# Performance work log

Hardware: AMD Instinct MI355X
Metric: run time of the kernel (lower is better)

The kernel has to match this reference:

```python
import jax, jax.numpy as jnp
import numpy as np

N = 100000   # nodes
E = 400000   # edges
G = 1024     # graphs in batch
IN = 4; H = 128; HD = 4; DH = H // HD; L = 3; ED = 4; FF = 2 * H; JK = H * L
SCALE = 1.0 / np.sqrt(DH).astype(np.float32)


def _ln(x, g, b):
    m = x.mean(-1, keepdims=True)
    v = x.var(-1, keepdims=True)
    return (x - m) / jnp.sqrt(v + 1e-5) * g + b


def setup_inputs() -> dict:
    key = jax.random.key(0)
    ks = jax.random.split(key, 24)
    rn = lambda k, s, sc=0.05: jax.random.normal(k, s, jnp.float32) * sc
    return {
        "x": rn(ks[0], (N, IN), 1.0),
        "edge_index": jax.random.randint(ks[1], (2, E), 0, N),
        "edge_attr": rn(ks[2], (E, ED), 1.0),
        "batch": jnp.sort(jax.random.randint(ks[3], (N,), 0, G)),
        "u": rn(ks[4], (G, 1), 1.0),
        "Win": rn(ks[5], (IN, H)), "b_in": jnp.zeros(H),
        "Wq": rn(ks[6], (L, H, H)), "bq": jnp.zeros((L, H)),
        "Wk": rn(ks[7], (L, H, H)), "bk": jnp.zeros((L, H)),
        "Wv": rn(ks[8], (L, H, H)), "bv": jnp.zeros((L, H)),
        "We": rn(ks[9], (L, ED, H)),
        "Wskip": rn(ks[10], (L, H, H)), "bskip": jnp.zeros((L, H)),
        "ln1_g": jnp.ones((L, H)), "ln1_b": jnp.zeros((L, H)),
        "Wf1": rn(ks[11], (L, H, FF)), "bf1": jnp.zeros((L, FF)),
        "Wf2": rn(ks[12], (L, FF, H)), "bf2": jnp.zeros((L, H)),
        "ln2_g": jnp.ones((L, H)), "ln2_b": jnp.zeros((L, H)),
        "Wg1": rn(ks[13], (JK, H)), "bg1": jnp.zeros(H),
        "Wg2": rn(ks[14], (H, 1)), "bg2": jnp.zeros(1),
        "Wh1": rn(ks[15], (JK + 1, H)), "bh1": jnp.zeros(H),
        "Wh2": rn(ks[16], (H, 3)), "bh2": jnp.zeros(3),
    }


def reference(x, edge_index, edge_attr, batch, u,
              Win, b_in, Wq, bq, Wk, bk, Wv, bv, We, Wskip, bskip,
              ln1_g, ln1_b, Wf1, bf1, Wf2, bf2, ln2_g, ln2_b,
              Wg1, bg1, Wg2, bg2, Wh1, bh1, Wh2, bh2):
    src, dst = edge_index[0], edge_index[1]
    h = x @ Win + b_in                                   # [N,H]
    xs = []
    for l in range(L):
        q = (h @ Wq[l] + bq[l]).reshape(N, HD, DH)
        k_n = h @ Wk[l] + bk[l]
        v_n = h @ Wv[l] + bv[l]
        e = edge_attr @ We[l]                            # [E,H] edge bias
        ke = (k_n[src] + e).reshape(E, HD, DH)
        ve = (v_n[src] + e).reshape(E, HD, DH)
        logits = (q[dst] * ke).sum(-1) * SCALE           # [E,HD]
        m = jax.ops.segment_max(logits, dst, N)
        p = jnp.exp(logits - m[dst])
        s = jax.ops.segment_sum(p, dst, N)
        alpha = p / (s[dst] + 1e-16)                     # segment softmax per dst node
        agg = jax.ops.segment_sum(alpha[:, :, None] * ve, dst, N).reshape(N, H)
        attn = agg + h @ Wskip[l] + bskip[l]             # root weight (skip lin)
        h = _ln(h + attn, ln1_g[l], ln1_b[l])
        ff = jax.nn.relu(h @ Wf1[l] + bf1[l]) @ Wf2[l] + bf2[l]
        h = _ln(h + ff, ln2_g[l], ln2_b[l])
        xs.append(h)
    xc = jnp.concatenate(xs, -1)                         # JumpingKnowledge 'cat' [N,JK]
    gate = (jax.nn.relu(xc @ Wg1 + bg1) @ Wg2 + bg2)[:, 0]  # [N]
    gm = jax.ops.segment_max(gate, batch, G)
    gp = jnp.exp(gate - gm[batch])
    gs = jax.ops.segment_sum(gp, batch, G)
    w = gp / (gs[batch] + 1e-16)                         # per-graph softmax
    pooled = jax.ops.segment_sum(w[:, None] * xc, batch, G)  # [G,JK]
    out = jnp.concatenate([pooled, u], 1)                # [G,JK+1]
    return jax.nn.relu(out @ Wh1 + bh1) @ Wh2 + bh2      # [G,3]
```

## Files before the change

### kernel.cpp

```cpp
#include <hip/hip_runtime.h>
#include <math.h>

#define H 128
#define LAYERS 3
#define FFDIM 256
#define JK 384
#define ATT_SCALE 0.17677669529663687f

typedef unsigned short u16;
typedef __attribute__((ext_vector_type(4))) float f32x4;
typedef __attribute__((ext_vector_type(8))) short short8;
typedef __attribute__((ext_vector_type(8))) unsigned short ushort8v;

static inline int cdiv(int a, int b) { return (a + b - 1) / b; }

static __device__ __forceinline__ float bf2f(u16 u) {
    union { unsigned int i; float f; } v; v.i = ((unsigned int)u) << 16; return v.f;
}
static __device__ __forceinline__ u16 f2bf(float f) {
    union { float f; unsigned int i; } v; v.f = f;
    unsigned int r = v.i + 0x7FFFu + ((v.i >> 16) & 1u);
    return (u16)(r >> 16);
}

__global__ void hist_kernel(const int* __restrict__ ei, int* __restrict__ counts, int E) {
    int e = blockIdx.x * blockDim.x + threadIdx.x;
    if (e >= E) return;
    atomicAdd(&counts[ei[E + e]], 1);
}

__global__ __launch_bounds__(256) void scan1_kernel(const int* __restrict__ counts,
                                                    int* __restrict__ offsets,
                                                    int* __restrict__ bsum, int N) {
    __shared__ int sh[256];
    int t = threadIdx.x;
    int base = blockIdx.x * 1024 + t * 4;
    int v0 = 0, v1 = 0, v2 = 0, v3 = 0;
    if (base + 3 < N) {
        int4 q = *(const int4*)&counts[base];
        v0 = q.x; v1 = q.y; v2 = q.z; v3 = q.w;
    } else {
        if (base < N) v0 = counts[base];
        if (base + 1 < N) v1 = counts[base + 1];
        if (base + 2 < N) v2 = counts[base + 2];
        if (base + 3 < N) v3 = counts[base + 3];
    }
    int ts = v0 + v1 + v2 + v3;
    sh[t] = ts; __syncthreads();
    for (int off = 1; off < 256; off <<= 1) {
        int x = (t >= off) ? sh[t - off] : 0;
        __syncthreads(); sh[t] += x; __syncthreads();
    }
    int excl = sh[t] - ts;
    if (base < N)     offsets[base]     = excl;
    if (base + 1 < N) offsets[base + 1] = excl + v0;
    if (base + 2 < N) offsets[base + 2] = excl + v0 + v1;
    if (base + 3 < N) offsets[base + 3] = excl + v0 + v1 + v2;
    if (t == 255) bsum[blockIdx.x] = sh[255];
}

__global__ __launch_bounds__(128) void scan2_kernel(const int* __restrict__ bsum,
                                                    int* __restrict__ boffs,
                                                    int* __restrict__ offsets, int nb, int N) {
    __shared__ int sh[128];
    int t = threadIdx.x;
    int s = (t < nb) ? bsum[t] : 0;
    sh[t] = s; __syncthreads();
    for (int off = 1; off < 128; off <<= 1) {
        int x = (t >= off) ? sh[t - off] : 0;
        __syncthreads(); sh[t] += x; __syncthreads();
    }
    if (t < nb) boffs[t] = sh[t] - s;
    if (t == 0) offsets[N] = sh[nb - 1];
}

__global__ __launch_bounds__(256) void scan3_kernel(int* __restrict__ offsets,
                                                    const int* __restrict__ boffs, int N) {
    int add = boffs[blockIdx.x];
    int base = blockIdx.x * 1024 + threadIdx.x * 4;
#pragma unroll
    for (int i = 0; i < 4; ++i)
        if (base + i < N) offsets[base + i] += add;
}

__global__ void scatter_kernel(const int* __restrict__ ei, const float* __restrict__ eattr,
                               const int* __restrict__ offsets,
                               int* __restrict__ cursor, int* __restrict__ psrc,
                               float4* __restrict__ pe, int E) {
    int e = blockIdx.x * blockDim.x + threadIdx.x;
    if (e >= E) return;
    int d = ei[E + e];
    int pos = atomicAdd(&cursor[d], 1);
    int o = offsets[d] + pos;
    psrc[o] = ei[e];
    pe[o] = *(const float4*)&eattr[(size_t)e * 4];
}

__global__ __launch_bounds__(256) void dhist_kernel(const int* __restrict__ counts,
                                                    int* __restrict__ dhist, int N) {
    __shared__ int lh[64];
    int t = threadIdx.x;
    if (t < 64) lh[t] = 0;
    __syncthreads();
    int n = blockIdx.x * 256 + t;
    if (n < N) atomicAdd(&lh[min(counts[n], 63)], 1);
    __syncthreads();
    if (t < 64 && lh[t]) atomicAdd(&dhist[t], lh[t]);
}

__global__ __launch_bounds__(64) void dscan_kernel(const int* __restrict__ dhist,
                                                   int* __restrict__ dcur) {
    __shared__ int sh[64];
    int t = threadIdx.x;
    int s = dhist[t];
    sh[t] = s; __syncthreads();
    for (int off = 1; off < 64; off <<= 1) {
        int x = (t >= off) ? sh[t - off] : 0;
        __syncthreads(); sh[t] += x; __syncthreads();
    }
    dcur[t] = sh[t] - s;
}

__global__ __launch_bounds__(256) void dscatter_kernel(const int* __restrict__ counts,
                                                       int* __restrict__ dcur,
                                                       int* __restrict__ nperm, int N) {
    __shared__ int lh[64], lbase[64];
    int t = threadIdx.x;
    if (t < 64) lh[t] = 0;
    __syncthreads();
    int n = blockIdx.x * 256 + t;
    int b = 0, rank = 0;
    if (n < N) {
        b = min(counts[n], 63);
        rank = atomicAdd(&lh[b], 1);
    }
    __syncthreads();
    if (t < 64 && lh[t]) lbase[t] = atomicAdd(&dcur[t], lh[t]);
    __syncthreads();
    if (n < N) nperm[lbase[b] + rank] = n;
}

__global__ void graph_bounds_kernel(const int* __restrict__ batch, int* __restrict__ gstart,
                                    int N, int G) {
    int g = blockIdx.x * blockDim.x + threadIdx.x;
    if (g > G) return;
    int lo = 0, hi = N;
    while (lo < hi) { int mid = (lo + hi) >> 1; if (batch[mid] < g) lo = mid + 1; else hi = mid; }
    gstart[g] = lo;
}

struct TD { const float* src; int dstoff, K, N; };
struct TA { TD d[19]; };

__global__ __launch_bounds__(256) void wconv_kernel(TA a, u16* __restrict__ WT) {
    TD d = a.d[blockIdx.y];
    int i = blockIdx.x * 256 + threadIdx.x;
    int tot = d.K * d.N;
    if (i >= tot) return;
    int c = i / d.K, k = i - c * d.K;
    WT[d.dstoff + i] = f2bf(d.src[(size_t)k * d.N + c]);
}

__global__ __launch_bounds__(256) void input_proj_kernel(const float* __restrict__ x,
                                                         const float* __restrict__ Win,
                                                         const float* __restrict__ b_in,
                                                         u16* __restrict__ h, int ldh, int N) {
    int idx = blockIdx.x * 256 + threadIdx.x;
    int n = idx >> 6, c = (idx & 63) * 2;
    if (n >= N) return;
    float4 xv = *(const float4*)&x[(size_t)n * 4];
    float o0 = b_in[c]     + xv.x * Win[c]     + xv.y * Win[H + c]     + xv.z * Win[2 * H + c]     + xv.w * Win[3 * H + c];
    float o1 = b_in[c + 1] + xv.x * Win[c + 1] + xv.y * Win[H + c + 1] + xv.z * Win[2 * H + c + 1] + xv.w * Win[3 * H + c + 1];
    ushort2 s; s.x = f2bf(o0); s.y = f2bf(o1);
    *(ushort2*)&h[(size_t)n * ldh + c] = s;
}

__device__ __forceinline__ void stage_tile(const u16* __restrict__ g, int ld, int row0,
                                           int nrows, int kt, u16* __restrict__ sm, int t) {
#pragma unroll
    for (int i = 0; i < 4; ++i) {
        int f = i * 256 + t;
        int row = f >> 3, ck = f & 7;
        int n = row0 + row; if (n >= nrows) n = nrows - 1;
        uint4 v = *(const uint4*)(g + (size_t)n * ld + kt + ck * 8);
        int sw = ck ^ (row & 7);
        *(uint4*)(sm + row * 64 + sw * 8) = v;
    }
}

template <int MODE, int NBY>
__global__ __launch_bounds__(256) void gemm_mfma(
    const u16* __restrict__ A, int lda,
    const u16* __restrict__ WT, int K,
    const float* __restrict__ b0, const float* __restrict__ b1,
    const float* __restrict__ b2, const float* __restrict__ b3,
    u16* __restrict__ obf, u16* __restrict__ obf2, float* __restrict__ of32,
    int nrows)
{
    alignas(16) __shared__ char smemraw[33792];
    u16* Asm = (u16*)smemraw;
    u16* Bsm = (u16*)(smemraw + 16384);
    float* stage = (float*)smemraw;
    int t = threadIdx.x;
    int lane = t & 63, wid = t >> 6;
    int wr = wid >> 1, wc = wid & 1;

    int T = gridDim.x, id = blockIdx.x;
    int qd = T >> 3, rr = T & 7;
    int xcd = id & 7, pos = id >> 3;
    int swz = (xcd < rr ? xcd * (qd + 1) : rr * (qd + 1) + (xcd - rr) * qd) + pos;
    int by = swz & (NBY - 1);
    int row0 = (swz / NBY) * 128;

    const u16* WTb = WT + (size_t)by * 128 * K;

    f32x4 acc[4][4] = {};

    for (int kt = 0; kt < K; kt += 64) {
        stage_tile(A, lda, row0, nrows, kt, Asm, t);
        stage_tile(WTb, K, 0, 128, kt, Bsm, t);
        __syncthreads();
        int g = lane >> 4;
        int l15 = lane & 15;
#pragma unroll
        for (int kk = 0; kk < 2; ++kk) {
            int cb = kk * 4 + g;
            short8 af[4], bf[4];
#pragma unroll
            for (int mi = 0; mi < 4; ++mi) {
                int r = wr * 64 + mi * 16 + l15;
                af[mi] = *(const short8*)(Asm + r * 64 + ((cb ^ (r & 7)) * 8));
            }
#pragma unroll
            for (int nj = 0; nj < 4; ++nj) {
                int c = wc * 64 + nj * 16 + l15;
                bf[nj] = *(const short8*)(Bsm + c * 64 + ((cb ^ (c & 7)) * 8));
            }
#pragma unroll
            for (int mi = 0; mi < 4; ++mi)
#pragma unroll
                for (int nj = 0; nj < 4; ++nj)
                    acc[mi][nj] = __builtin_amdgcn_mfma_f32_16x16x32_bf16(af[mi], bf[nj], acc[mi][nj], 0, 0, 0);
        }
        __syncthreads();
    }

    int g = lane >> 4, l15 = lane & 15;

    if (MODE == 3) {
        float* gsum = (float*)Asm;
        float part[4][4];
#pragma unroll
        for (int mi = 0; mi < 4; ++mi)
#pragma unroll
            for (int r = 0; r < 4; ++r) part[mi][r] = 0.f;
#pragma unroll
        for (int nj = 0; nj < 4; ++nj) {
            int col = wc * 64 + nj * 16 + l15;
            float bb = b0[col];
            float w2 = b1[col];
#pragma unroll
            for (int mi = 0; mi < 4; ++mi)
#pragma unroll
                for (int r = 0; r < 4; ++r) {
                    float v = fmaxf(acc[mi][nj][r] + bb, 0.f);
                    part[mi][r] = fmaf(v, w2, part[mi][r]);
                }
        }
#pragma unroll
        for (int off = 1; off <= 8; off <<= 1)
#pragma unroll
            for (int mi = 0; mi < 4; ++mi)
#pragma unroll
                for (int r = 0; r < 4; ++r) part[mi][r] += __shfl_xor(part[mi][r], off);
        if (wc == 0 && l15 == 0) {
#pragma unroll
            for (int mi = 0; mi < 4; ++mi)
#pragma unroll
                for (int r = 0; r < 4; ++r)
                    gsum[wr * 64 + mi * 16 + g * 4 + r] = part[mi][r];
        }
        __syncthreads();
        if (wc == 1 && l15 == 0) {
            float bg2v = b2[0];
#pragma unroll
            for (int mi = 0; mi < 4; ++mi)
#pragma unroll
                for (int r = 0; r < 4; ++r) {
                    int lr = wr * 64 + mi * 16 + g * 4 + r;
                    int n = row0 + lr;
                    if (n < nrows) of32[n] = part[mi][r] + gsum[lr] + bg2v;
                }
        }
        return;
    }

    const float* bias = (by == 0) ? b0 : (by == 1) ? b1 : (by == 2) ? b2 : b3;
    u16* ob; int ldob;
    if (by < 3) { ob = obf + by * 128; ldob = 384; }
    else { ob = obf2; ldob = 128; }

#pragma unroll
    for (int p = 0; p < 2; ++p) {
        if (wr == p) {
#pragma unroll
            for (int nj = 0; nj < 4; ++nj) {
                int col = wc * 64 + nj * 16 + l15;
                float bb = bias[col];
#pragma unroll
                for (int mi = 0; mi < 4; ++mi)
#pragma unroll
                    for (int r = 0; r < 4; ++r)
                        stage[(mi * 16 + g * 4 + r) * 132 + col] = acc[mi][nj][r] + bb;
            }
        }
        __syncthreads();
#pragma unroll
        for (int it = 0; it < 4; ++it) {
            int lr = it * 16 + (t >> 4);
            int gr = row0 + p * 64 + lr;
            if (gr < nrows) {
                int c8 = (t & 15) * 8;
                ushort8v o;
                if (by == 3) {
                    ushort8v hv = *(const ushort8v*)&A[(size_t)gr * lda + c8];
#pragma unroll
                    for (int i = 0; i < 8; ++i) o[i] = f2bf(stage[lr * 132 + c8 + i] + bf2f(hv[i]));
                } else {
#pragma unroll
                    for (int i = 0; i < 8; ++i) o[i] = f2bf(stage[lr * 132 + c8 + i]);
                }
                *(ushort8v*)&ob[(size_t)gr * ldob + c8] = o;
            }
        }
        __syncthreads();
    }
}

__global__ __launch_bounds__(256) void ff_fused(
    const u16* __restrict__ qkv,
    const u16* __restrict__ W1T,
    const u16* __restrict__ W2T,
    const float* __restrict__ bias1,
    const float* __restrict__ bias2,
    const float* __restrict__ g2, const float* __restrict__ b2v,
    u16* __restrict__ xcout,
    int nrows)
{
    alignas(16) __shared__ char smem[57344];
    u16* ff1s = (u16*)smem;
    u16* ast  = (u16*)(smem + 32768);
    u16* bst  = (u16*)(smem + 40960);
    float* stage = (float*)smem;

    int t = threadIdx.x;
    int lane = t & 63, wid = t >> 6;
    int wr = wid >> 1, wc = wid & 1;
    int g = lane >> 4, l15 = lane & 15;

    int T = gridDim.x, id = blockIdx.x;
    int qd = T >> 3, rr = T & 7;
    int xcd = id & 7, pos = id >> 3;
    int swz = (xcd < rr ? xcd * (qd + 1) : rr * (qd + 1) + (xcd - rr) * qd) + pos;
    int row0 = swz * 64;

    for (int ch = 0; ch < 2; ++ch) {
        f32x4 acc[2][4] = {};
        for (int kt = 0; kt < 128; kt += 64) {
#pragma unroll
            for (int i = 0; i < 2; ++i) {
                int f = i * 256 + t;
                int row = f >> 3, ck = f & 7;
                int n = row0 + row; if (n >= nrows) n = nrows - 1;
                uint4 v = *(const uint4*)(qkv + (size_t)n * 384 + kt + ck * 8);
                *(uint4*)(ast + row * 64 + ((ck ^ (row & 7)) * 8)) = v;
            }
#pragma unroll
            for (int i = 0; i < 4; ++i) {
                int f = i * 256 + t;
                int row = f >> 3, ck = f & 7;
                uint4 v = *(const uint4*)(W1T + (size_t)(ch * 128 + row) * 128 + kt + ck * 8);
                *(uint4*)(bst + row * 64 + ((ck ^ (row & 7)) * 8)) = v;
            }
            __syncthreads();
#pragma unroll
            for (int kk = 0; kk < 2; ++kk) {
                int cb = kk * 4 + g;
                short8 af[2], bf[4];
#pragma unroll
                for (int mi = 0; mi < 2; ++mi) {
                    int r = wr * 32 + mi * 16 + l15;
                    af[mi] = *(const short8*)(ast + r * 64 + ((cb ^ (r & 7)) * 8));
                }
#pragma unroll
                for (int nj = 0; nj < 4; ++nj) {
                    int c = wc * 64 + nj * 16 + l15;
                    bf[nj] = *(const short8*)(bst + c * 64 + ((cb ^ (c & 7)) * 8));
                }
#pragma unroll
                for (int mi = 0; mi < 2; ++mi)
#pragma unroll
                    for (int nj = 0; nj < 4; ++nj)
                        acc[mi][nj] = __builtin_amdgcn_mfma_f32_16x16x32_bf16(af[mi], bf[nj], acc[mi][nj], 0, 0, 0);
            }
            __syncthreads();
        }
#pragma unroll
        for (int nj = 0; nj < 4; ++nj) {
            int col = ch * 128 + wc * 64 + nj * 16 + l15;
            float bb = bias1[col];
            int cb2 = col >> 3, j = col & 7;
#pragma unroll
            for (int mi = 0; mi < 2; ++mi)
#pragma unroll
                for (int r = 0; r < 4; ++r) {
                    int row = wr * 32 + mi * 16 + g * 4 + r;
                    float v = fmaxf(acc[mi][nj][r] + bb, 0.f);
                    int sc = (cb2 & 24) | ((cb2 & 7) ^ (row & 7));
                    ff1s[row * 256 + sc * 8 + j] = f2bf(v);
                }
        }
    }

    f32x4 acc2[2][4] = {};
    for (int kt2 = 0; kt2 < 256; kt2 += 64) {
#pragma unroll
        for (int i = 0; i < 4; ++i) {
            int f = i * 256 + t;
            int row = f >> 3, ck = f & 7;
            uint4 v = *(const uint4*)(W2T + (size_t)row * 256 + kt2 + ck * 8);
            *(uint4*)(bst + row * 64 + ((ck ^ (row & 7)) * 8)) = v;
        }
        __syncthreads();
#pragma unroll
        for (int kk = 0; kk < 2; ++kk) {
            int cb = kk * 4 + g;
            short8 af[2], bf[4];
#pragma unroll
            for (int mi = 0; mi < 2; ++mi) {
                int r = wr * 32 + mi * 16 + l15;
                int sc = (kt2 >> 3) | (cb ^ (r & 7));
                af[mi] = *(const short8*)(ff1s + r * 256 + sc * 8);
            }
#pragma unroll
            for (int nj = 0; nj < 4; ++nj) {
                int c = wc * 64 + nj * 16 + l15;
                bf[nj] = *(const short8*)(bst + c * 64 + ((cb ^ (c & 7)) * 8));
            }
#pragma unroll
            for (int mi = 0; mi < 2; ++mi)
#pragma unroll
                for (int nj = 0; nj < 4; ++nj)
                    acc2[mi][nj] = __builtin_amdgcn_mfma_f32_16x16x32_bf16(af[mi], bf[nj], acc2[mi][nj], 0, 0, 0);
        }
        __syncthreads();
    }

#pragma unroll
    for (int nj = 0; nj < 4; ++nj) {
        int col = wc * 64 + nj * 16 + l15;
        float bb = bias2[col];
#pragma unroll
        for (int mi = 0; mi < 2; ++mi)
#pragma unroll
            for (int r = 0; r < 4; ++r) {
                int row = wr * 32 + mi * 16 + g * 4 + r;
                stage[row * 132 + col] = acc2[mi][nj][r] + bb;
            }
    }
    __syncthreads();
    int sub2 = t & 15, rowg = t >> 4;
#pragma unroll
    for (int it = 0; it < 4; ++it) {
        int lr = it * 16 + rowg;
        int gr = row0 + lr;
        bool ok = gr < nrows;
        int c8 = sub2 * 8;
        float tv[8]; float sum = 0.f, sq = 0.f;
        if (ok) {
            ushort8v rv = *(const ushort8v*)&qkv[(size_t)gr * 384 + c8];
#pragma unroll
            for (int i = 0; i < 8; ++i) {
                tv[i] = stage[lr * 132 + c8 + i] + bf2f(rv[i]);
                sum += tv[i]; sq += tv[i] * tv[i];
            }
        }
#pragma unroll
        for (int off = 1; off <= 8; off <<= 1) { sum += __shfl_xor(sum, off); sq += __shfl_xor(sq, off); }
        if (ok) {
            float mean = sum * (1.f / 128.f);
            float var = sq * (1.f / 128.f) - mean * mean;
            float rstd = rsqrtf(var + 1e-5f);
            ushort8v o;
#pragma unroll
            for (int i = 0; i < 8; ++i)
                o[i] = f2bf((tv[i] - mean) * rstd * g2[c8 + i] + b2v[c8 + i]);
            *(ushort8v*)&xcout[(size_t)gr * 384 + c8] = o;
        }
    }
}

__global__ __launch_bounds__(256) void attn_kernel(
    u16* __restrict__ qkv,
    const u16* __restrict__ skipb,
    const int* __restrict__ offsets,
    const int* __restrict__ nperm,
    const int* __restrict__ psrc, const float4* __restrict__ pe,
    const float* __restrict__ We_l,
    const float* __restrict__ g1, const float* __restrict__ b1,
    int N)
{
    int tid = threadIdx.x;
    int grp = tid >> 4;
    int sub = tid & 15;
    int idx = blockIdx.x * 16 + grp;
    if (idx >= N) return;
    int n = nperm[idx];
    int d0 = sub * 8;

    float we[4][8];
#pragma unroll
    for (int aa = 0; aa < 4; ++aa) {
        float4 w0 = *(const float4*)&We_l[aa * H + d0];
        float4 w1 = *(const float4*)&We_l[aa * H + d0 + 4];
        we[aa][0] = w0.x; we[aa][1] = w0.y; we[aa][2] = w0.z; we[aa][3] = w0.w;
        we[aa][4] = w1.x; we[aa][5] = w1.y; we[aa][6] = w1.z; we[aa][7] = w1.w;
    }

    ushort8v qraw = *(const ushort8v*)&qkv[(size_t)n * JK + d0];
    float qf[8];
#pragma unroll
    for (int i = 0; i < 8; ++i) qf[i] = bf2f(qraw[i]);

    float qe[4];
#pragma unroll
    for (int aa = 0; aa < 4; ++aa) {
        float s = 0.f;
#pragma unroll
        for (int i = 0; i < 8; ++i) s = fmaf(qf[i], we[aa][i], s);
        s += __shfl_xor(s, 1);
        s += __shfl_xor(s, 2);
        qe[aa] = s;
    }

    float m0 = -INFINITY, ss0 = 0.f, m1 = -INFINITY, ss1 = 0.f;
    float a0[8] = {}, a1[8] = {};
    float w0a = 0.f, w0b = 0.f, w0c = 0.f, w0d = 0.f;
    float w1a = 0.f, w1b = 0.f, w1c = 0.f, w1d = 0.f;
    int e0v = offsets[n], e1v = offsets[n + 1];
    int deg = e1v - e0v;
    int npairs = deg >> 1;

    if (npairs > 0) {
        int j0 = e0v;
        int sA = psrc[j0], sB = psrc[j0 + 1];
        float4 eaA = pe[j0], eaB = pe[j0 + 1];
        const u16* srA = qkv + (size_t)sA * JK;
        const u16* srB = qkv + (size_t)sB * JK;
        ushort8v krA = *(const ushort8v*)&srA[H + d0];
        ushort8v vrA = *(const ushort8v*)&srA[2 * H + d0];
        ushort8v krB = *(const ushort8v*)&srB[H + d0];
        ushort8v vrB = *(const ushort8v*)&srB[2 * H + d0];
        for (int it = 0; it < npairs; ++it) {
            float4 eaA2, eaB2; ushort8v krA2, vrA2, krB2, vrB2;
            if (it + 1 < npairs) {
                int jn = e0v + (it + 1) * 2;
                int sA2 = psrc[jn], sB2 = psrc[jn + 1];
                eaA2 = pe[jn]; eaB2 = pe[jn + 1];
                const u16* srA2 = qkv + (size_t)sA2 * JK;
                const u16* srB2 = qkv + (size_t)sB2 * JK;
                krA2 = *(const ushort8v*)&srA2[H + d0];
                vrA2 = *(const ushort8v*)&srA2[2 * H + d0];
                krB2 = *(const ushort8v*)&srB2[H + d0];
                vrB2 = *(const ushort8v*)&srB2[2 * H + d0];
            }
            float pA = 0.f, pB = 0.f;
#pragma unroll
            for (int i = 0; i < 8; ++i) {
                pA = fmaf(qf[i], bf2f(krA[i]), pA);
                pB = fmaf(qf[i], bf2f(krB[i]), pB);
            }
            pA += __shfl_xor(pA, 1); pB += __shfl_xor(pB, 1);
            pA += __shfl_xor(pA, 2); pB += __shfl_xor(pB, 2);
            float lgA = (pA + eaA.x * qe[0] + eaA.y * qe[1] + eaA.z * qe[2] + eaA.w * qe[3]) * ATT_SCALE;
            float lgB = (pB + eaB.x * qe[0] + eaB.y * qe[1] + eaB.z * qe[2] + eaB.w * qe[3]) * ATT_SCALE;
            float mnA = fmaxf(m0, lgA);
            float mnB = fmaxf(m1, lgB);
            float cA = __expf(m0 - mnA), cB = __expf(m1 - mnB);
            float pvA = __expf(lgA - mnA), pvB = __expf(lgB - mnB);
            ss0 = ss0 * cA + pvA;
            ss1 = ss1 * cB + pvB;
#pragma unroll
            for (int i = 0; i < 8; ++i) {
                a0[i] = a0[i] * cA + pvA * bf2f(vrA[i]);
                a1[i] = a1[i] * cB + pvB * bf2f(vrB[i]);
            }
            w0a = w0a * cA + pvA * eaA.x; w0b = w0b * cA + pvA * eaA.y;
            w0c = w0c * cA + pvA * eaA.z; w0d = w0d * cA + pvA * eaA.w;
            w1a = w1a * cB + pvB * eaB.x; w1b = w1b * cB + pvB * eaB.y;
            w1c = w1c * cB + pvB * eaB.z; w1d = w1d * cB + pvB * eaB.w;
            m0 = mnA; m1 = mnB;
            krA = krA2; vrA = vrA2; eaA = eaA2;
            krB = krB2; vrB = vrB2; eaB = eaB2;
        }
    }
    if (deg & 1) {
        int j = e1v - 1;
        int s = psrc[j];
        float4 ea = pe[j];
        const u16* sr = qkv + (size_t)s * JK;
        ushort8v kr = *(const ushort8v*)&sr[H + d0];
        ushort8v vr = *(const ushort8v*)&sr[2 * H + d0];
        float part = 0.f;
#pragma unroll
        for (int i = 0; i < 8; ++i) part = fmaf(qf[i], bf2f(kr[i]), part);
        part += __shfl_xor(part, 1);
        part += __shfl_xor(part, 2);
        float lg = (part + ea.x * qe[0] + ea.y * qe[1] + ea.z * qe[2] + ea.w * qe[3]) * ATT_SCALE;
        float mn = fmaxf(m0, lg);
        float c = __expf(m0 - mn);
        float pv = __expf(lg - mn);
        ss0 = ss0 * c + pv;
#pragma unroll
        for (int i = 0; i < 8; ++i) a0[i] = a0[i] * c + pv * bf2f(vr[i]);
        w0a = w0a * c + pv * ea.x; w0b = w0b * c + pv * ea.y;
        w0c = w0c * c + pv * ea.z; w0d = w0d * c + pv * ea.w;
        m0 = mn;
    }
    float mm = fmaxf(m0, m1);
    if (mm > -INFINITY) {
        float c0 = (m0 > -INFINITY) ? __expf(m0 - mm) : 0.f;
        float c1 = (m1 > -INFINITY) ? __expf(m1 - mm) : 0.f;
        ss0 = ss0 * c0 + ss1 * c1;
#pragma unroll
        for (int i = 0; i < 8; ++i) a0[i] = a0[i] * c0 + a1[i] * c1;
        w0a = w0a * c0 + w1a * c1; w0b = w0b * c0 + w1b * c1;
        w0c = w0c * c0 + w1c * c1; w0d = w0d * c0 + w1d * c1;
    }
    float inv = 1.f / (ss0 + 1e-16f);
#pragma unroll
    for (int i = 0; i < 8; ++i)
        a0[i] += w0a * we[0][i] + w0b * we[1][i] + w0c * we[2][i] + w0d * we[3][i];

    ushort8v skraw = *(const ushort8v*)&skipb[(size_t)n * H + d0];
    float tv[8], sum = 0.f, sq = 0.f;
#pragma unroll
    for (int i = 0; i < 8; ++i) {
        tv[i] = a0[i] * inv + bf2f(skraw[i]);
        sum += tv[i]; sq += tv[i] * tv[i];
    }
#pragma unroll
    for (int off = 1; off <= 8; off <<= 1) { sum += __shfl_xor(sum, off); sq += __shfl_xor(sq, off); }
    float mean = sum * (1.f / 128.f);
    float var = sq * (1.f / 128.f) - mean * mean;
    float rstd = rsqrtf(var + 1e-5f);
    float4 ga = *(const float4*)&g1[d0];
    float4 gb = *(const float4*)&g1[d0 + 4];
    float4 ba = *(const float4*)&b1[d0];
    float4 bb = *(const float4*)&b1[d0 + 4];
    float gg[8] = {ga.x, ga.y, ga.z, ga.w, gb.x, gb.y, gb.z, gb.w};
    float bbv[8] = {ba.x, ba.y, ba.z, ba.w, bb.x, bb.y, bb.z, bb.w};
    ushort8v obv;
#pragma unroll
    for (int i = 0; i < 8; ++i)
        obv[i] = f2bf((tv[i] - mean) * rstd * gg[i] + bbv[i]);
    *(ushort8v*)&qkv[(size_t)n * JK + d0] = obv;
}

#define PCH 512
__global__ __launch_bounds__(256) void pool_kernel(const float* __restrict__ gate,
                                                   const u16* __restrict__ xc,
                                                   const int* __restrict__ gstart,
                                                   const float* __restrict__ u,
                                                   float* __restrict__ pooled, int G) {
    int g = blockIdx.x;
    int t = threadIdx.x;
    int s0 = gstart[g], s1 = gstart[g + 1];
    __shared__ float red[256];
    __shared__ float w[PCH];
    float mx = -INFINITY;
    for (int i = s0 + t; i < s1; i += 256) mx = fmaxf(mx, gate[i]);
    red[t] = mx; __syncthreads();
    for (int off = 128; off; off >>= 1) { if (t < off) red[t] = fmaxf(red[t], red[t + off]); __syncthreads(); }
    float gm = red[0]; __syncthreads();
    float sm = 0.f;
    for (int i = s0 + t; i < s1; i += 256) sm += __expf(gate[i] - gm);
    red[t] = sm; __syncthreads();
    for (int off = 128; off; off >>= 1) { if (t < off) red[t] += red[t + off]; __syncthreads(); }
    float inv = 1.f / (red[0] + 1e-16f);
    float acc0 = 0.f, acc1 = 0.f;
    for (int base = s0; base < s1; base += PCH) {
        int cnt = min(PCH, s1 - base);
        __syncthreads();
        for (int i = t; i < cnt; i += 256) w[i] = __expf(gate[base + i] - gm) * inv;
        __syncthreads();
        for (int c = 0; c < cnt; ++c) {
            const u16* row = xc + (size_t)(base + c) * JK;
            float wc = w[c];
            acc0 = fmaf(wc, bf2f(row[t]), acc0);
            if (t < 128) acc1 = fmaf(wc, bf2f(row[t + 256]), acc1);
        }
    }
    pooled[(size_t)g * (JK + 1) + t] = acc0;
    if (t < 128) pooled[(size_t)g * (JK + 1) + t + 256] = acc1;
    if (t == 0) pooled[(size_t)g * (JK + 1) + JK] = u[g];
}

__global__ __launch_bounds__(128) void head_kernel(const float* __restrict__ pooled,
                                                   const float* __restrict__ Wh1,
                                                   const float* __restrict__ bh1,
                                                   const float* __restrict__ Wh2,
                                                   const float* __restrict__ bh2,
                                                   float* __restrict__ out, int G) {
    int g = blockIdx.x;
    int j = threadIdx.x;
    __shared__ float hid[128];
    float acc = bh1[j];
    const float* pr = pooled + (size_t)g * (JK + 1);
    for (int k = 0; k < JK + 1; ++k) acc = fmaf(pr[k], Wh1[(size_t)k * H + j], acc);
    hid[j] = fmaxf(acc, 0.f);
    __syncthreads();
    if (j < 3) {
        float o = bh2[j];
        for (int k = 0; k < H; ++k) o += hid[k] * Wh2[k * 3 + j];
        out[(size_t)g * 3 + j] = o;
    }
}

extern "C" void kernel_launch(void* const* d_in, const int* in_sizes, int n_in,
                              void* d_out, int out_size, void* d_ws, size_t ws_size,
                              hipStream_t stream) {
    const float* x     = (const float*)d_in[0];
    const int*   ei    = (const int*)d_in[1];
    const float* eattr = (const float*)d_in[2];
    const int*   batch = (const int*)d_in[3];
    const float* u     = (const float*)d_in[4];
    const float* Win   = (const float*)d_in[5];
    const float* b_in  = (const float*)d_in[6];
    const float* Wq    = (const float*)d_in[7];
    const float* bq    = (const float*)d_in[8];
    const float* Wk    = (const float*)d_in[9];
    const float* bk    = (const float*)d_in[10];
    const float* Wv    = (const float*)d_in[11];
    const float* bv    = (const float*)d_in[12];
    const float* We    = (const float*)d_in[13];
    const float* Wskip = (const float*)d_in[14];
    const float* bskip = (const float*)d_in[15];
    const float* ln1_g = (const float*)d_in[16];
    const float* ln1_b = (const float*)d_in[17];
    const float* Wf1   = (const float*)d_in[18];
    const float* bf1   = (const float*)d_in[19];
    const float* Wf2   = (const float*)d_in[20];
    const float* bf2   = (const float*)d_in[21];
    const float* ln2_g = (const float*)d_in[22];
    const float* ln2_b = (const float*)d_in[23];
    const float* Wg1   = (const float*)d_in[24];
    const float* bg1   = (const float*)d_in[25];
    const float* Wg2   = (const float*)d_in[26];
    const float* bg2   = (const float*)d_in[27];
    const float* Wh1   = (const float*)d_in[28];
    const float* bh1   = (const float*)d_in[29];
    const float* Wh2   = (const float*)d_in[30];
    const float* bh2   = (const float*)d_in[31];

    const int N = in_sizes[3];
    const int E = in_sizes[1] / 2;
    const int G = in_sizes[4];

    char* p = (char*)d_ws;
    auto alloc = [&](size_t bytes) { char* r = p; p += (bytes + 255) & ~(size_t)255; return r; };
    int*    counts  = (int*)alloc((size_t)N * 4);
    int*    cursor  = (int*)alloc((size_t)N * 4);
    int*    offsets = (int*)alloc((size_t)(N + 1) * 4);
    int*    psrc    = (int*)alloc((size_t)E * 4);
    float4* pe      = (float4*)alloc((size_t)E * 16);
    int*    nperm   = (int*)alloc((size_t)N * 4);
    int*    gstart  = (int*)alloc((size_t)(G + 1) * 4);
    int*    bsum    = (int*)alloc(128 * 4);
    int*    boffs   = (int*)alloc(128 * 4);
    int*    dhist   = (int*)alloc(64 * 4);
    int*    dcur    = (int*)alloc(64 * 4);
    float*  gate    = (float*)alloc((size_t)N * 4);
    float*  pooled  = (float*)alloc((size_t)G * (JK + 1) * 4);
    u16*    WT      = (u16*)alloc((size_t)442368 * 2);
    u16*    skipb   = (u16*)alloc((size_t)N * H * 2);
    u16*    xc      = (u16*)alloc((size_t)N * JK * 2);
    u16*    qkv     = (u16*)alloc((size_t)N * JK * 2);

    const int QKVS_OFF = 0;
    const int F1_OFF   = 3 * 65536;
    const int F2_OFF   = F1_OFF + 3 * 32768;
    const int G1_OFF   = F2_OFF + 3 * 32768;

    hipMemsetAsync(counts, 0, (size_t)N * 4, stream);
    hipMemsetAsync(cursor, 0, (size_t)N * 4, stream);
    hipMemsetAsync(dhist, 0, 64 * 4, stream);

    int eb = cdiv(E, 256);
    int nb = cdiv(N, 1024);
    int nthb = cdiv(N, 256);
    hist_kernel<<<eb, 256, 0, stream>>>(ei, counts, E);
    scan1_kernel<<<nb, 256, 0, stream>>>(counts, offsets, bsum, N);
    scan2_kernel<<<1, 128, 0, stream>>>(bsum, boffs, offsets, nb, N);
    scan3_kernel<<<nb, 256, 0, stream>>>(offsets, boffs, N);
    scatter_kernel<<<eb, 256, 0, stream>>>(ei, eattr, offsets, cursor, psrc, pe, E);
    dhist_kernel<<<nthb, 256, 0, stream>>>(counts, dhist, N);
    dscan_kernel<<<1, 64, 0, stream>>>(dhist, dcur);
    dscatter_kernel<<<nthb, 256, 0, stream>>>(counts, dcur, nperm, N);
    graph_bounds_kernel<<<cdiv(G + 1, 256), 256, 0, stream>>>(batch, gstart, N, G);

    TA ta;
    for (int l = 0; l < 3; ++l) {
        ta.d[l * 4 + 0] = { Wq    + (size_t)l * 16384, QKVS_OFF + l * 65536 + 0,     128, 128 };
        ta.d[l * 4 + 1] = { Wk    + (size_t)l * 16384, QKVS_OFF + l * 65536 + 16384, 128, 128 };
        ta.d[l * 4 + 2] = { Wv    + (size_t)l * 16384, QKVS_OFF + l * 65536 + 32768, 128, 128 };
        ta.d[l * 4 + 3] = { Wskip + (size_t)l * 16384, QKVS_OFF + l * 65536 + 49152, 128, 128 };
        ta.d[12 + l]    = { Wf1   + (size_t)l * 32768, F1_OFF   + l * 32768,         128, 256 };
        ta.d[15 + l]    = { Wf2   + (size_t)l * 32768, F2_OFF   + l * 32768,         256, 128 };
    }
    ta.d[18] = { Wg1, G1_OFF, 384, 128 };
    dim3 wg(cdiv(49152, 256), 19);
    wconv_kernel<<<wg, 256, 0, stream>>>(ta, WT);

    input_proj_kernel<<<cdiv(N * 64, 256), 256, 0, stream>>>(x, Win, b_in, xc, JK, N);

    int gb = cdiv(N, 128);
    int gb64 = cdiv(N, 64);
    int nb16 = cdiv(N, 16);
    for (int l = 0; l < LAYERS; ++l) {
        const u16* hin = xc + (size_t)((l == 0) ? 0 : (l - 1) * H);
        gemm_mfma<0, 4><<<gb * 4, 256, 0, stream>>>(
            hin, JK, WT + QKVS_OFF + (size_t)l * 65536, 128,
            bq + l * H, bk + l * H, bv + l * H, bskip + l * H,
            qkv, skipb, nullptr, N);
        attn_kernel<<<nb16, 256, 0, stream>>>(qkv, skipb, offsets, nperm, psrc, pe,
                                              We + (size_t)l * 4 * H, ln1_g + l * H, ln1_b + l * H,
                                              N);
        ff_fused<<<gb64, 256, 0, stream>>>(
            qkv, WT + F1_OFF + (size_t)l * 32768, WT + F2_OFF + (size_t)l * 32768,
            bf1 + (size_t)l * FFDIM, bf2 + (size_t)l * H,
            ln2_g + (size_t)l * H, ln2_b + (size_t)l * H,
            xc + (size_t)l * H, N);
    }

    gemm_mfma<3, 1><<<gb, 256, 0, stream>>>(
        xc, JK, WT + G1_OFF, JK,
        bg1, Wg2, bg2, nullptr,
        nullptr, nullptr, gate, N);
    pool_kernel<<<G, 256, 0, stream>>>(gate, xc, gstart, u, pooled, G);
    head_kernel<<<G, 128, 0, stream>>>(pooled, Wh1, bh1, Wh2, bh2, (float*)d_out, G);
}
```

Baseline: 609.9 us.

## Fuse Q/K/V/skip projections into one block per row tile reusing A

The QKV+skip GEMM now launches one block per 128-row tile that loads the full A tile (K=128) into shared memory once and loops over the four weight column blocks, instead of launching four blocks that each reload A. The skip residual is read from the staged shared A tile rather than global memory, and the epilogue staging buffer uses an XOR swizzle with vectorized float4 reads instead of padded scalar reads. The gate GEMM is split out into its own kernel. This cuts redundant A loads and the grid is four times smaller, which may reduce parallelism and latency hiding.

```diff
diff --git a/kernel.cpp b/kernel.cpp
--- a/kernel.cpp
+++ b/kernel.cpp
@@ -188,40 +188,139 @@
     }
 }
 
-template <int MODE, int NBY>
-__global__ __launch_bounds__(256) void gemm_mfma(
+__global__ __launch_bounds__(256) void qkvs_kernel(
     const u16* __restrict__ A, int lda,
-    const u16* __restrict__ WT, int K,
-    const float* __restrict__ b0, const float* __restrict__ b1,
-    const float* __restrict__ b2, const float* __restrict__ b3,
-    u16* __restrict__ obf, u16* __restrict__ obf2, float* __restrict__ of32,
-    int nrows)
+    const u16* __restrict__ WT,
+    const float* __restrict__ bq, const float* __restrict__ bk,
+    const float* __restrict__ bv, const float* __restrict__ bs,
+    u16* __restrict__ qkv, u16* __restrict__ skipb, int nrows)
 {
-    alignas(16) __shared__ char smemraw[33792];
-    u16* Asm = (u16*)smemraw;
-    u16* Bsm = (u16*)(smemraw + 16384);
-    float* stage = (float*)smemraw;
+    alignas(16) __shared__ u16 Asm[2][128 * 64];
+    alignas(16) __shared__ u16 Bsm[2][128 * 64];
+    float* stage = (float*)Bsm;
     int t = threadIdx.x;
     int lane = t & 63, wid = t >> 6;
     int wr = wid >> 1, wc = wid & 1;
+    int g = lane >> 4, l15 = lane & 15;
 
     int T = gridDim.x, id = blockIdx.x;
     int qd = T >> 3, rr = T & 7;
     int xcd = id & 7, pos = id >> 3;
     int swz = (xcd < rr ? xcd * (qd + 1) : rr * (qd + 1) + (xcd - rr) * qd) + pos;
-    int by = swz & (NBY - 1);
-    int row0 = (swz / NBY) * 128;
-
-    const u16* WTb = WT + (size_t)by * 128 * K;
+    int row0 = swz * 128;
+
+    stage_tile(A, lda, row0, nrows, 0,  Asm[0], t);
+    stage_tile(A, lda, row0, nrows, 64, Asm[1], t);
+
+    for (int by = 0; by < 4; ++by) {
+        const u16* WTb = WT + (size_t)by * 128 * 128;
+        stage_tile(WTb, 128, 0, 128, 0,  Bsm[0], t);
+        stage_tile(WTb, 128, 0, 128, 64, Bsm[1], t);
+        __syncthreads();
+
+        f32x4 acc[4][4] = {};
+#pragma unroll
+        for (int h = 0; h < 2; ++h) {
+#pragma unroll
+            for (int kk = 0; kk < 2; ++kk) {
+                int cb = kk * 4 + g;
+                short8 af[4], bf[4];
+#pragma unroll
+                for (int mi = 0; mi < 4; ++mi) {
+                    int r = wr * 64 + mi * 16 + l15;
+                    af[mi] = *(const short8*)(Asm[h] + r * 64 + ((cb ^ (r & 7)) * 8));
+                }
+#pragma unroll
+                for (int nj = 0; nj < 4; ++nj) {
+                    int c = wc * 64 + nj * 16 + l15;
+                    bf[nj] = *(const short8*)(Bsm[h] + c * 64 + ((cb ^ (c & 7)) * 8));
+                }
+#pragma unroll
+                for (int mi = 0; mi < 4; ++mi)
+#pragma unroll
+                    for (int nj = 0; nj < 4; ++nj)
+                        acc[mi][nj] = __builtin_amdgcn_mfma_f32_16x16x32_bf16(af[mi], bf[nj], acc[mi][nj], 0, 0, 0);
+            }
+        }
+        __syncthreads();
+
+        const float* bias = (by == 0) ? bq : (by == 1) ? bk : (by == 2) ? bv : bs;
+        u16* ob; int ldob;
+        if (by < 3) { ob = qkv + by * 128; ldob = 384; }
+        else { ob = skipb; ldob = 128; }
+
+#pragma unroll
+        for (int p = 0; p < 2; ++p) {
+            if (wr == p) {
+#pragma unroll
+                for (int nj = 0; nj < 4; ++nj) {
+                    int col = wc * 64 + nj * 16 + l15;
+                    float bb = bias[col];
+#pragma unroll
+                    for (int mi = 0; mi < 4; ++mi)
+#pragma unroll
+                        for (int r = 0; r < 4; ++r) {
+                            int lr = mi * 16 + g * 4 + r;
+                            stage[lr * 128 + (col ^ ((lr & 7) << 3))] = acc[mi][nj][r] + bb;
+                        }
+                }
+            }
+            __syncthreads();
+#pragma unroll
+            for (int it = 0; it < 4; ++it) {
+                int lr = it * 16 + (t >> 4);
+                int gr = row0 + p * 64 + lr;
+                if (gr < nrows) {
+                    int c8 = (t & 15) * 8;
+                    int sc = c8 ^ ((lr & 7) << 3);
+                    float4 va = *(float4*)&stage[lr * 128 + sc];
+                    float4 vb = *(float4*)&stage[lr * 128 + sc + 4];
+                    float vv[8] = {va.x, va.y, va.z, va.w, vb.x, vb.y, vb.z, vb.w};
+                    ushort8v o;
+                    if (by == 3) {
+                        int arow = p * 64 + lr;
+                        int cc = t & 15;
+                        int h2 = cc >> 3, ck = cc & 7;
+                        ushort8v hv = *(const ushort8v*)(Asm[h2] + arow * 64 + ((ck ^ (arow & 7)) * 8));
+#pragma unroll
+                        for (int i = 0; i < 8; ++i) o[i] = f2bf(vv[i] + bf2f(hv[i]));
+                    } else {
+#pragma unroll
+                        for (int i = 0; i < 8; ++i) o[i] = f2bf(vv[i]);
+                    }
+                    *(ushort8v*)&ob[(size_t)gr * ldob + c8] = o;
+                }
+            }
+            __syncthreads();
+        }
+    }
+}
+
+__global__ __launch_bounds__(256) void gate_kernel(
+    const u16* __restrict__ A, int lda,
+    const u16* __restrict__ WT, int K,
+    const float* __restrict__ bg1, const float* __restrict__ Wg2,
+    const float* __restrict__ bg2,
+    float* __restrict__ gate, int nrows)
+{
+    alignas(16) __shared__ u16 Asm[128 * 64];
+    alignas(16) __shared__ u16 Bsm[128 * 64];
+    int t = threadIdx.x;
+    int lane = t & 63, wid = t >> 6;
+    int wr = wid >> 1, wc = wid & 1;
+    int g = lane >> 4, l15 = lane & 15;
+
+    int T = gridDim.x, id = blockIdx.x;
+    int qd = T >> 3, rr = T & 7;
+    int xcd = id & 7, pos = id >> 3;
+    int swz = (xcd < rr ? xcd * (qd + 1) : rr * (qd + 1) + (xcd - rr) * qd) + pos;
+    int row0 = swz * 128;
 
     f32x4 acc[4][4] = {};
-
     for (int kt = 0; kt < K; kt += 64) {
         stage_tile(A, lda, row0, nrows, kt, Asm, t);
-        stage_tile(WTb, K, 0, 128, kt, Bsm, t);
+        stage_tile(WT, K, 0, 128, kt, Bsm, t);
         __syncthreads();
-        int g = lane >> 4;
-        int l15 = lane & 15;
 #pragma unroll
         for (int kk = 0; kk < 2; ++kk) {
             int cb = kk * 4 + g;
@@ -245,95 +344,49 @@
         __syncthreads();
     }
 
-    int g = lane >> 4, l15 = lane & 15;
-
-    if (MODE == 3) {
-        float* gsum = (float*)Asm;
-        float part[4][4];
+    float* gsum = (float*)Asm;
+    float part[4][4];
+#pragma unroll
+    for (int mi = 0; mi < 4; ++mi)
+#pragma unroll
+        for (int r = 0; r < 4; ++r) part[mi][r] = 0.f;
+#pragma unroll
+    for (int nj = 0; nj < 4; ++nj) {
+        int col = wc * 64 + nj * 16 + l15;
+        float bb = bg1[col];
+        float w2 = Wg2[col];
 #pragma unroll
         for (int mi = 0; mi < 4; ++mi)
 #pragma unroll
-            for (int r = 0; r < 4; ++r) part[mi][r] = 0.f;
-#pragma unroll
-        for (int nj = 0; nj < 4; ++nj) {
-            int col = wc * 64 + nj * 16 + l15;
-            float bb = b0[col];
-            float w2 = b1[col];
-#pragma unroll
-            for (int mi = 0; mi < 4; ++mi)
-#pragma unroll
-                for (int r = 0; r < 4; ++r) {
-                    float v = fmaxf(acc[mi][nj][r] + bb, 0.f);
-                    part[mi][r] = fmaf(v, w2, part[mi][r]);
-                }
-        }
-#pragma unroll
-        for (int off = 1; off <= 8; off <<= 1)
-#pragma unroll
-            for (int mi = 0; mi < 4; ++mi)
-#pragma unroll
-                for (int r = 0; r < 4; ++r) part[mi][r] += __shfl_xor(part[mi][r], off);
-        if (wc == 0 && l15 == 0) {
-#pragma unroll
-            for (int mi = 0; mi < 4; ++mi)
-#pragma unroll
-                for (int r = 0; r < 4; ++r)
-                    gsum[wr * 64 + mi * 16 + g * 4 + r] = part[mi][r];
-        }
-        __syncthreads();
-        if (wc == 1 && l15 == 0) {
-            float bg2v = b2[0];
-#pragma unroll
-            for (int mi = 0; mi < 4; ++mi)
-#pragma unroll
-                for (int r = 0; r < 4; ++r) {
-                    int lr = wr * 64 + mi * 16 + g * 4 + r;
-                    int n = row0 + lr;
-                    if (n < nrows) of32[n] = part[mi][r] + gsum[lr] + bg2v;
-                }
-        }
-        return;
-    }
-
-    const float* bias = (by == 0) ? b0 : (by == 1) ? b1 : (by == 2) ? b2 : b3;
-    u16* ob; int ldob;
-    if (by < 3) { ob = obf + by * 128; ldob = 384; }
-    else { ob = obf2; ldob = 128; }
-
-#pragma unroll
-    for (int p = 0; p < 2; ++p) {
-        if (wr == p) {
-#pragma unroll
-            for (int nj = 0; nj < 4; ++nj) {
-                int col = wc * 64 + nj * 16 + l15;
-                float bb = bias[col];
-#pragma unroll
-                for (int mi = 0; mi < 4; ++mi)
-#pragma unroll
-                    for (int r = 0; r < 4; ++r)
-                        stage[(mi * 16 + g * 4 + r) * 132 + col] = acc[mi][nj][r] + bb;
-            }
-        }
-        __syncthreads();
-#pragma unroll
-        for (int it = 0; it < 4; ++it) {
-            int lr = it * 16 + (t >> 4);
-            int gr = row0 + p * 64 + lr;
-            if (gr < nrows) {
-                int c8 = (t & 15) * 8;
-                ushort8v o;
-                if (by == 3) {
-                    ushort8v hv = *(const ushort8v*)&A[(size_t)gr * lda + c8];
-#pragma unroll
-                    for (int i = 0; i < 8; ++i) o[i] = f2bf(stage[lr * 132 + c8 + i] + bf2f(hv[i]));
-                } else {
-#pragma unroll
-                    for (int i = 0; i < 8; ++i) o[i] = f2bf(stage[lr * 132 + c8 + i]);
-                }
-                *(ushort8v*)&ob[(size_t)gr * ldob + c8] = o;
-            }
-        }
-        __syncthreads();
+            for (int r = 0; r < 4; ++r) {
+                float v = fmaxf(acc[mi][nj][r] + bb, 0.f);
+                part[mi][r] = fmaf(v, w2, part[mi][r]);
+            }
+    }
+#pragma unroll
+    for (int off = 1; off <= 8; off <<= 1)
+#pragma unroll
+        for (int mi = 0; mi < 4; ++mi)
+#pragma unroll
+            for (int r = 0; r < 4; ++r) part[mi][r] += __shfl_xor(part[mi][r], off);
+    if (wc == 0 && l15 == 0) {
+#pragma unroll
+        for (int mi = 0; mi < 4; ++mi)
+#pragma unroll
+            for (int r = 0; r < 4; ++r)
+                gsum[wr * 64 + mi * 16 + g * 4 + r] = part[mi][r];
+    }
+    __syncthreads();
+    if (wc == 1 && l15 == 0) {
+        float bg2v = bg2[0];
+#pragma unroll
+        for (int mi = 0; mi < 4; ++mi)
+#pragma unroll
+            for (int r = 0; r < 4; ++r) {
+                int lr = wr * 64 + mi * 16 + g * 4 + r;
+                int n = row0 + lr;
+                if (n < nrows) gate[n] = part[mi][r] + gsum[lr] + bg2v;
+            }
     }
 }
 
@@ -829,10 +882,10 @@
     int nb16 = cdiv(N, 16);
     for (int l = 0; l < LAYERS; ++l) {
         const u16* hin = xc + (size_t)((l == 0) ? 0 : (l - 1) * H);
-        gemm_mfma<0, 4><<<gb * 4, 256, 0, stream>>>(
-            hin, JK, WT + QKVS_OFF + (size_t)l * 65536, 128,
+        qkvs_kernel<<<gb, 256, 0, stream>>>(
+            hin, JK, WT + QKVS_OFF + (size_t)l * 65536,
             bq + l * H, bk + l * H, bv + l * H, bskip + l * H,
-            qkv, skipb, nullptr, N);
+            qkv, skipb, N);
         attn_kernel<<<nb16, 256, 0, stream>>>(qkv, skipb, offsets, nperm, psrc, pe,
                                               We + (size_t)l * 4 * H, ln1_g + l * H, ln1_b + l * H,
                                               N);
@@ -843,10 +896,7 @@
             xc + (size_t)l * H, N);
     }
 
-    gemm_mfma<3, 1><<<gb, 256, 0, stream>>>(
-        xc, JK, WT + G1_OFF, JK,
-        bg1, Wg2, bg2, nullptr,
-        nullptr, nullptr, gate, N);
+    gate_kernel<<<gb, 256, 0, stream>>>(xc, JK, WT + G1_OFF, JK, bg1, Wg2, bg2, gate, N);
     pool_kernel<<<G, 256, 0, stream>>>(gate, xc, gstart, u, pooled, G);
     head_kernel<<<G, 128, 0, stream>>>(pooled, Wh1, bh1, Wh2, bh2, (float*)d_out, G);
 }
```

Result: slower. 674.6 us (+10.6%).
